# Performance work log

Measured on AMD Instinct MI355X. Metric: run time of the kernel, lower is better.

The kernel has to match this reference:

```python
import jax, jax.numpy as jnp
import numpy as np

EPS = 1e-8
N_ITER = 3
S = 8      # n_slots
D = 64     # slot_size
HID = 128  # mlp hidden


def _ln(x, w, b):
    m = jnp.mean(x, axis=-1, keepdims=True)
    v = jnp.var(x, axis=-1, keepdims=True)
    return (x - m) * jax.lax.rsqrt(v + 1e-5) * w + b


def setup_inputs() -> dict:
    key = jax.random.key(0)
    ks = jax.random.split(key, 20)
    B, N, Din = 128, 4096, 64
    g = lambda k, sh, s: (jax.random.normal(k, sh, jnp.float32) * s)
    return {
        "inputs": jax.random.normal(ks[0], (B, N, Din), jnp.float32),
        "eps_noise": jax.random.normal(ks[1], (B, S, D), jnp.float32),
        "slot_mu": g(ks[2], (1, 1, D), 0.1),
        "slot_logvar": g(ks[3], (1, 1, D), 0.1),
        "k_w": g(ks[4], (D, Din), 1.0 / np.sqrt(Din)),
        "v_w": g(ks[5], (D, Din), 1.0 / np.sqrt(Din)),
        "q_w": g(ks[6], (D, D), 1.0 / np.sqrt(D)),
        "ni_w": jnp.ones((Din,), jnp.float32), "ni_b": jnp.zeros((Din,), jnp.float32),
        "ns_w": jnp.ones((D,), jnp.float32),  "ns_b": jnp.zeros((D,), jnp.float32),
        "nr_w": jnp.ones((D,), jnp.float32),  "nr_b": jnp.zeros((D,), jnp.float32),
        "gru_wih": g(ks[7], (3 * D, D), 1.0 / np.sqrt(D)),
        "gru_whh": g(ks[8], (3 * D, D), 1.0 / np.sqrt(D)),
        "gru_bih": jnp.zeros((3 * D,), jnp.float32),
        "gru_bhh": jnp.zeros((3 * D,), jnp.float32),
        "mlp_w1": g(ks[9], (HID, D), 1.0 / np.sqrt(D)),
        "mlp_w2": g(ks[10], (D, HID), 1.0 / np.sqrt(HID)),
        "mlp_b2": jnp.zeros((D,), jnp.float32),
    }


def _gru(x, h, wih, whh, bih, bhh):
    gi = x @ wih.T + bih  # [BS, 3D]
    gh = h @ whh.T + bhh
    i_r, i_z, i_n = jnp.split(gi, 3, axis=-1)
    h_r, h_z, h_n = jnp.split(gh, 3, axis=-1)
    r = jax.nn.sigmoid(i_r + h_r)
    z = jax.nn.sigmoid(i_z + h_z)
    n = jnp.tanh(i_n + r * h_n)
    return (1.0 - z) * n + z * h


def _step(slots, k, v, q_w, ns_w, ns_b, nr_w, nr_b,
          gru_wih, gru_whh, gru_bih, gru_bhh, mlp_w1, mlp_w2, mlp_b2):
    B = slots.shape[0]
    q = _ln(slots, ns_w, ns_b) @ q_w.T                     # [B,S,D]
    logits = jnp.einsum('bnd,bsd->bns', k, q)              # [B,N,S]
    w = jax.nn.softmax(logits, axis=-1) + EPS              # softmax over slots
    w = w / jnp.sum(w, axis=-2, keepdims=True)             # renorm over tokens
    atten_maps = jnp.einsum('bns,bnd->bsd', w, v)          # [B,S,D]
    h = _gru(atten_maps.reshape(B * S, D), slots.reshape(B * S, D),
             gru_wih, gru_whh, gru_bih, gru_bhh)
    h = h + (jax.nn.relu(_ln(h, nr_w, nr_b) @ mlp_w1.T) @ mlp_w2.T + mlp_b2)
    return h.reshape(B, S, D), w


def reference(inputs, eps_noise, slot_mu, slot_logvar, k_w, v_w, q_w,
              ni_w, ni_b, ns_w, ns_b, nr_w, nr_b,
              gru_wih, gru_whh, gru_bih, gru_bhh, mlp_w1, mlp_w2, mlp_b2):
    std = jnp.exp(0.5 * slot_logvar)
    slots = slot_mu + std * eps_noise                      # [B,S,D]
    x = _ln(inputs, ni_w, ni_b)
    k = (x @ k_w.T) / np.sqrt(D).astype(np.float32)        # [B,N,D]
    v = x @ v_w.T
    args = (q_w, ns_w, ns_b, nr_w, nr_b, gru_wih, gru_whh,
            gru_bih, gru_bhh, mlp_w1, mlp_w2, mlp_b2)
    for _ in range(N_ITER):
        slots, w = _step(slots, k, v, *args)
    slots, w = _step(jax.lax.stop_gradient(slots), k, v, *args)
    return slots, w
```

## Files before the change

### kernel.cpp

```cpp
#include <hip/hip_runtime.h>
#include <hip/hip_bf16.h>

#define BB 128
#define NN 4096
#define DD 64
#define SS 8
#define HH 128

typedef __attribute__((ext_vector_type(8))) short short8;
typedef __attribute__((ext_vector_type(4))) float f32x4;

__device__ __forceinline__ float warp_red_sum(float v) {
    #pragma unroll
    for (int off = 32; off; off >>= 1) v += __shfl_xor(v, off);
    return v;
}

__device__ __forceinline__ float bcastlane(float v, int l) {
    return __int_as_float(__builtin_amdgcn_readlane(__float_as_int(v), l));
}

__device__ __forceinline__ unsigned short bfu(float f) {
    __hip_bfloat16 h = __float2bfloat16(f);
    return *(unsigned short*)&h;
}

__device__ __forceinline__ unsigned pk2(float a, float b) {
    return (unsigned)bfu(a) | ((unsigned)bfu(b) << 16);
}

__global__ __launch_bounds__(256) void prep_kernel(
    const float* __restrict__ v_w, const float* __restrict__ q_w,
    const float* __restrict__ wih, const float* __restrict__ whh,
    const float* __restrict__ w1, const float* __restrict__ w2,
    float* __restrict__ vwT, float* __restrict__ qwT,
    float* __restrict__ wihT, float* __restrict__ whhT,
    float* __restrict__ w1T, float* __restrict__ w2T)
{
    int i0 = blockIdx.x * blockDim.x + threadIdx.x;
    int nthr = gridDim.x * blockDim.x;
    for (int t = i0; t < 4096; t += nthr) {
        int i = t >> 6, o = t & 63;
        vwT[t] = v_w[o * 64 + i];
        qwT[t] = q_w[o * 64 + i];
    }
    for (int t = i0; t < 12288; t += nthr) {
        int r = t / 192, c = t % 192;
        wihT[t] = wih[c * 64 + r];
        whhT[t] = whh[c * 64 + r];
    }
    for (int t = i0; t < 8192; t += nthr) {
        int r = t >> 7, c = t & 127;
        w1T[t] = w1[c * 64 + r];
    }
    for (int t = i0; t < 8192; t += nthr) {
        int r = t >> 6, c = t & 63;
        w2T[t] = w2[c * 128 + r];
    }
}

__global__ __launch_bounds__(256) void init_q_kernel(
    const float* __restrict__ eps, const float* __restrict__ mu,
    const float* __restrict__ lv, const float* __restrict__ qwT,
    const float* __restrict__ k_w,
    const float* __restrict__ nsw, const float* __restrict__ nsb,
    float* __restrict__ slots, unsigned short* __restrict__ qb,
    float* __restrict__ zbuf)
{
    const int tid = threadIdx.x, lane = tid & 63;
    const int row = blockIdx.x * 4 + (tid >> 6);
    const int idx = row * 64 + lane;
    float s0 = mu[lane] + __expf(0.5f * lv[lane]) * eps[idx];
    slots[idx] = s0;
    float m = warp_red_sum(s0) * (1.0f / 64.0f);
    float dx = s0 - m;
    float var = warp_red_sum(dx * dx) * (1.0f / 64.0f);
    float xln = dx * rsqrtf(var + 1e-5f) * nsw[lane] + nsb[lane];
    float q = 0.f;
    #pragma unroll 8
    for (int i = 0; i < 64; ++i) q = fmaf(bcastlane(xln, i), qwT[i * 64 + lane], q);
    float qp = 0.f;
    #pragma unroll 8
    for (int o = 0; o < 64; ++o) qp = fmaf(bcastlane(q, o), k_w[o * 64 + lane], qp);
    qb[idx] = bfu(qp * 0.125f);
    int g = blockIdx.x * 256 + tid;
    for (int j = g; j < 66560; j += 65536) zbuf[j] = 0.f;
}

__global__ __launch_bounds__(256) void phase_a_ln(
    const float* __restrict__ inp, const float* __restrict__ niw, const float* __restrict__ nib,
    unsigned short* __restrict__ xb, unsigned short* __restrict__ xbt)
{
    __shared__ unsigned short xt[64 * 136];
    const int tid = threadIdx.x, lane = tid & 63, widx = tid >> 6;
    const int tg = lane >> 4, dq = lane & 15;
    const float4 wni = *(const float4*)&niw[dq * 4];
    const float4 bni = *(const float4*)&nib[dq * 4];
    const int tok0 = blockIdx.x * 128;
    const int sw = dq & 7;
    #pragma unroll
    for (int it = 0; it < 8; ++it) {
        const int m = widx * 32 + it * 4 + tg;
        float4 x = *(const float4*)&inp[(size_t)(tok0 + m) * 64 + dq * 4];
        float s1 = x.x + x.y + x.z + x.w;
        float s2 = fmaf(x.x, x.x, fmaf(x.y, x.y, fmaf(x.z, x.z, x.w * x.w)));
        #pragma unroll
        for (int o = 1; o < 16; o <<= 1) { s1 += __shfl_xor(s1, o); s2 += __shfl_xor(s2, o); }
        float mean = s1 * (1.0f / 64.0f);
        float var = s2 * (1.0f / 64.0f) - mean * mean;
        float rstd = rsqrtf(var + 1e-5f);
        float y0 = (x.x - mean) * rstd * wni.x + bni.x;
        float y1 = (x.y - mean) * rstd * wni.y + bni.y;
        float y2 = (x.z - mean) * rstd * wni.z + bni.z;
        float y3 = (x.w - mean) * rstd * wni.w + bni.w;
        uint2 p; p.x = pk2(y0, y1); p.y = pk2(y2, y3);
        *(uint2*)&xb[(size_t)(tok0 + m) * 64 + dq * 4] = p;
        const int col = ((((m >> 3) ^ sw) << 3) | (m & 7));
        xt[(dq * 4 + 0) * 136 + col] = bfu(y0);
        xt[(dq * 4 + 1) * 136 + col] = bfu(y1);
        xt[(dq * 4 + 2) * 136 + col] = bfu(y2);
        xt[(dq * 4 + 3) * 136 + col] = bfu(y3);
    }
    __syncthreads();
    const int b = blockIdx.x >> 5, tin = (blockIdx.x & 31) * 128;
    const int d = tid >> 2, q4 = tid & 3;
    const int sr = (d >> 2) & 7;
    #pragma unroll
    for (int c = 0; c < 4; ++c) {
        const int cc = q4 * 4 + c;
        uint4 o = *(uint4*)&xt[d * 136 + ((cc ^ sr) << 3)];
        *(uint4*)&xbt[((size_t)b * 64 + d) * 4096 + tin + cc * 8] = o;
    }
}

__global__ __launch_bounds__(256) void attn_mfma(
    const __hip_bfloat16* __restrict__ xb, const unsigned short* __restrict__ xbt,
    const unsigned short* __restrict__ qb,
    float* __restrict__ numer, float* __restrict__ denom, float* __restrict__ wout)
{
    __shared__ unsigned short smem[24192];
    unsigned short* Qs = smem;
    const int tid = threadIdx.x, lane = tid & 63, widx = tid >> 6;
    unsigned short* wls = smem + 1152 + widx * 1152;
    unsigned short* vt  = smem + 5760 + widx * 4608;
    const int b = blockIdx.y;

    for (int t = tid; t < 1024; t += 256) {
        int s = t >> 6, dd = t & 63;
        Qs[s * 72 + dd] = (s < 8) ? qb[b * 512 + t] : (unsigned short)0;
    }
    for (int t = lane; t < 576; t += 64) wls[576 + t] = 0;
    __syncthreads();

    const int quad = lane >> 4, l16 = lane & 15;
    short8 aq0 = *(const short8*)&Qs[l16 * 72 + quad * 8];
    short8 aq1 = *(const short8*)&Qs[l16 * 72 + 32 + quad * 8];

    f32x4 accv[4];
    #pragma unroll
    for (int nt = 0; nt < 4; ++nt) accv[nt] = (f32x4){0.f, 0.f, 0.f, 0.f};
    float dacc[4] = {0.f, 0.f, 0.f, 0.f};

    const int twave0 = blockIdx.x * 512 + widx * 128;
    const int vd = lane >> 3, vc = (lane & 7) * 8;
    #pragma unroll
    for (int iter = 0; iter < 2; ++iter) {
        const int t0 = twave0 + iter * 64;
        uint4 vld[8];
        #pragma unroll
        for (int i = 0; i < 8; ++i)
            vld[i] = *(const uint4*)&xbt[((size_t)b * 64 + i * 8 + vd) * 4096 + t0 + vc];

        #pragma unroll
        for (int t4 = 0; t4 < 4; ++t4) {
            const int tok = t0 + t4 * 16 + l16;
            const size_t xrow = ((size_t)b * NN + tok) * 64;
            short8 bk0 = *(const short8*)&xb[xrow + quad * 8];
            short8 bk1 = *(const short8*)&xb[xrow + 32 + quad * 8];
            f32x4 lg = (f32x4){0.f, 0.f, 0.f, 0.f};
            lg = __builtin_amdgcn_mfma_f32_16x16x32_bf16(aq0, bk0, lg, 0, 0, 0);
            lg = __builtin_amdgcn_mfma_f32_16x16x32_bf16(aq1, bk1, lg, 0, 0, 0);
            float e[4];
            #pragma unroll
            for (int r = 0; r < 4; ++r) e[r] = __expf(lg[r]);
            float s4 = (e[0] + e[1]) + (e[2] + e[3]);
            float stot = s4 + __shfl_xor(s4, 16);
            float rs = __builtin_amdgcn_rcpf(stot);
            float wv[4];
            #pragma unroll
            for (int r = 0; r < 4; ++r) { wv[r] = fmaf(e[r], rs, 1e-8f); dacc[r] += wv[r]; }
            if (quad < 2) {
                #pragma unroll
                for (int r = 0; r < 4; ++r)
                    wls[(quad * 4 + r) * 72 + t4 * 16 + l16] = bfu(wv[r]);
                if (wout)
                    *(float4*)&wout[((size_t)b * NN + tok) * 8 + quad * 4] =
                        make_float4(wv[0], wv[1], wv[2], wv[3]);
            }
        }
        #pragma unroll
        for (int i = 0; i < 8; ++i)
            *(uint4*)&vt[(i * 8 + vd) * 72 + vc] = vld[i];
        #pragma unroll
        for (int ks = 0; ks < 2; ++ks) {
            short8 aw = *(const short8*)&wls[l16 * 72 + ks * 32 + quad * 8];
            #pragma unroll
            for (int nt = 0; nt < 4; ++nt) {
                short8 bv = *(const short8*)&vt[(nt * 16 + l16) * 72 + ks * 32 + quad * 8];
                accv[nt] = __builtin_amdgcn_mfma_f32_16x16x32_bf16(aw, bv, accv[nt], 0, 0, 0);
            }
        }
    }
    #pragma unroll
    for (int r = 0; r < 4; ++r) {
        dacc[r] += __shfl_xor(dacc[r], 1);
        dacc[r] += __shfl_xor(dacc[r], 2);
        dacc[r] += __shfl_xor(dacc[r], 4);
        dacc[r] += __shfl_xor(dacc[r], 8);
    }
    __syncthreads();
    float* red = (float*)(smem + 5760);
    float* dred = red + 2048;
    if (quad < 2) {
        #pragma unroll
        for (int nt = 0; nt < 4; ++nt)
            #pragma unroll
            for (int r = 0; r < 4; ++r)
                red[widx * 512 + (quad * 4 + r) * 64 + nt * 16 + l16] = accv[nt][r];
        if (l16 == 0) {
            #pragma unroll
            for (int r = 0; r < 4; ++r) dred[widx * 8 + quad * 4 + r] = dacc[r];
        }
    }
    __syncthreads();
    for (int e = tid; e < 512; e += 256)
        atomicAdd(numer + (size_t)b * 512 + e, red[e] + red[512 + e] + red[1024 + e] + red[1536 + e]);
    if (tid < 8)
        atomicAdd(denom + b * 8 + tid, dred[tid] + dred[8 + tid] + dred[16 + tid] + dred[24 + tid]);
}

__global__ __launch_bounds__(256) void gru_q_kernel(
    const float* __restrict__ numerX, const float* __restrict__ denom,
    const float* __restrict__ slotsIn,
    const float* __restrict__ vwT, const float* __restrict__ wihT, const float* __restrict__ whhT,
    const float* __restrict__ w1T, const float* __restrict__ w2T,
    const float* __restrict__ bih, const float* __restrict__ bhh,
    const float* __restrict__ nrw, const float* __restrict__ nrb,
    const float* __restrict__ b2,
    const float* __restrict__ qwT, const float* __restrict__ k_w,
    const float* __restrict__ nsw, const float* __restrict__ nsb,
    float* __restrict__ slotsOut, unsigned short* __restrict__ qb,
    float* __restrict__ zbuf)
{
    const int tid = threadIdx.x, lane = tid & 63;
    const int row = blockIdx.x * 4 + (tid >> 6);
    float nx = numerX[row * 64 + lane];
    float xp = 0.f;
    #pragma unroll 8
    for (int i = 0; i < 64; ++i) xp = fmaf(bcastlane(nx, i), vwT[i * 64 + lane], xp);
    float x = xp / denom[row];
    float h = slotsIn[row * 64 + lane];
    float air = 0, aiz = 0, ain = 0, ahr = 0, ahz = 0, ahn = 0;
    #pragma unroll 8
    for (int i = 0; i < 64; ++i) {
        float xi = bcastlane(x, i), hi = bcastlane(h, i);
        const float* wi = wihT + i * 192;
        const float* wh = whhT + i * 192;
        air = fmaf(xi, wi[lane], air);
        aiz = fmaf(xi, wi[64 + lane], aiz);
        ain = fmaf(xi, wi[128 + lane], ain);
        ahr = fmaf(hi, wh[lane], ahr);
        ahz = fmaf(hi, wh[64 + lane], ahz);
        ahn = fmaf(hi, wh[128 + lane], ahn);
    }
    air += bih[lane]; aiz += bih[64 + lane]; ain += bih[128 + lane];
    ahr += bhh[lane]; ahz += bhh[64 + lane]; ahn += bhh[128 + lane];
    float r = 1.f / (1.f + __expf(-(air + ahr)));
    float z = 1.f / (1.f + __expf(-(aiz + ahz)));
    float n = tanhf(ain + r * ahn);
    float hn = (1.f - z) * n + z * h;
    float m = warp_red_sum(hn) * (1.0f / 64.0f);
    float dx = hn - m;
    float var = warp_red_sum(dx * dx) * (1.0f / 64.0f);
    float u = dx * rsqrtf(var + 1e-5f) * nrw[lane] + nrb[lane];
    float o0 = 0.f, o1 = 0.f;
    #pragma unroll 8
    for (int i = 0; i < 64; ++i) {
        float ui = bcastlane(u, i);
        const float* w1r = w1T + i * 128;
        o0 = fmaf(ui, w1r[lane], o0);
        o1 = fmaf(ui, w1r[64 + lane], o1);
    }
    o0 = fmaxf(o0, 0.f); o1 = fmaxf(o1, 0.f);
    float y = 0.f;
    #pragma unroll 8
    for (int j = 0; j < 64; ++j) y = fmaf(bcastlane(o0, j), w2T[j * 64 + lane], y);
    #pragma unroll 8
    for (int j = 0; j < 64; ++j) y = fmaf(bcastlane(o1, j), w2T[(64 + j) * 64 + lane], y);
    y += b2[lane];
    float out = hn + y;
    slotsOut[row * 64 + lane] = out;
    float m2 = warp_red_sum(out) * (1.0f / 64.0f);
    float dx2 = out - m2;
    float var2 = warp_red_sum(dx2 * dx2) * (1.0f / 64.0f);
    float u2 = dx2 * rsqrtf(var2 + 1e-5f) * nsw[lane] + nsb[lane];
    float q = 0.f;
    #pragma unroll 8
    for (int i = 0; i < 64; ++i) q = fmaf(bcastlane(u2, i), qwT[i * 64 + lane], q);
    float qp = 0.f;
    #pragma unroll 8
    for (int o = 0; o < 64; ++o) qp = fmaf(bcastlane(q, o), k_w[o * 64 + lane], qp);
    qb[row * 64 + lane] = bfu(qp * 0.125f);
    int g = blockIdx.x * 256 + tid;
    for (int j = g; j < 66560; j += 65536) zbuf[j] = 0.f;
}

__global__ __launch_bounds__(256) void renorm_kernel(float* __restrict__ wout,
                                                     const float* __restrict__ denom)
{
    const size_t i4 = (size_t)blockIdx.x * blockDim.x + threadIdx.x;
    const size_t b = i4 >> 13;
    const int half = (int)(i4 & 1);
    float4 v = reinterpret_cast<float4*>(wout)[i4];
    const float4 dv = reinterpret_cast<const float4*>(denom)[b * 2 + half];
    v.x /= dv.x; v.y /= dv.y; v.z /= dv.z; v.w /= dv.w;
    reinterpret_cast<float4*>(wout)[i4] = v;
}

extern "C" void kernel_launch(void* const* d_in, const int* in_sizes, int n_in,
                              void* d_out, int out_size, void* d_ws, size_t ws_size,
                              hipStream_t stream)
{
    const float* inputs  = (const float*)d_in[0];
    const float* eps_n   = (const float*)d_in[1];
    const float* mu      = (const float*)d_in[2];
    const float* lv      = (const float*)d_in[3];
    const float* k_w     = (const float*)d_in[4];
    const float* v_w     = (const float*)d_in[5];
    const float* q_w     = (const float*)d_in[6];
    const float* ni_w    = (const float*)d_in[7];
    const float* ni_b    = (const float*)d_in[8];
    const float* ns_w    = (const float*)d_in[9];
    const float* ns_b    = (const float*)d_in[10];
    const float* nr_w    = (const float*)d_in[11];
    const float* nr_b    = (const float*)d_in[12];
    const float* gru_wih = (const float*)d_in[13];
    const float* gru_whh = (const float*)d_in[14];
    const float* gru_bih = (const float*)d_in[15];
    const float* gru_bhh = (const float*)d_in[16];
    const float* mlp_w1  = (const float*)d_in[17];
    const float* mlp_w2  = (const float*)d_in[18];
    const float* mlp_b2  = (const float*)d_in[19];

    char* wsb = (char*)d_ws;
    unsigned short* xb  = (unsigned short*)wsb;
    unsigned short* xbt = (unsigned short*)(wsb + 67108864);
    float* f      = (float*)(wsb + 134217728);
    float* slotsA = f;
    float* slotsB = f + 65536;
    unsigned short* qb = (unsigned short*)(f + 131072);
    float* numer0 = f + 163840;
    float* denom0 = f + 229376;
    float* numer1 = f + 230400;
    float* denom1 = f + 295936;
    float* vwT    = f + 296960;
    float* qwT    = f + 301056;
    float* wihT   = f + 305152;
    float* whhT   = f + 317440;
    float* w1T    = f + 329728;
    float* w2T    = f + 337920;

    float* out_slots = (float*)d_out;
    float* out_w     = out_slots + 65536;

    prep_kernel<<<64, 256, 0, stream>>>(v_w, q_w, gru_wih, gru_whh, mlp_w1, mlp_w2,
                                        vwT, qwT, wihT, whhT, w1T, w2T);
    init_q_kernel<<<256, 256, 0, stream>>>(eps_n, mu, lv, qwT, k_w, ns_w, ns_b,
                                           slotsA, qb, numer0);
    phase_a_ln<<<4096, 256, 0, stream>>>(inputs, ni_w, ni_b, xb, xbt);

    float* cur = slotsA;
    float* numers[2] = {numer0, numer1};
    float* denoms[2] = {denom0, denom1};
    for (int step = 0; step < 4; ++step) {
        int pb = step & 1;
        attn_mfma<<<dim3(8, 128), 256, 0, stream>>>((const __hip_bfloat16*)xb, xbt, qb,
                                                    numers[pb], denoms[pb],
                                                    step == 3 ? out_w : nullptr);
        float* nxt = (step == 3) ? out_slots : ((step & 1) ? slotsA : slotsB);
        gru_q_kernel<<<256, 256, 0, stream>>>(numers[pb], denoms[pb], cur,
                                              vwT, wihT, whhT, w1T, w2T,
                                              gru_bih, gru_bhh, nr_w, nr_b, mlp_b2,
                                              qwT, k_w, ns_w, ns_b,
                                              nxt, qb, numers[1 - pb]);
        cur = nxt;
    }
    renorm_kernel<<<4096, 256, 0, stream>>>(out_w, denom1);
}
```

Baseline: 448.1 us.

## Load V fragments straight into MFMA registers and widen per-thread LayerNorm vectors

The attention kernel now loads each wave's transposed V tile from global memory directly into MFMA B-operand registers instead of staging it through shared memory. This removes the LDS write/read round trip and shrinks the kernel's static LDS footprint, which may allow more blocks per CU. The price is narrower contiguous runs per row in the global loads. Separately, the input LayerNorm kernel has each thread handle 8 features with two float4 loads and one 16-byte bf16 store, reducing the shuffle rounds. The LDS transpose swizzle is widened to 16 chunk positions to match the new write pattern.

```diff
diff --git a/kernel.cpp b/kernel.cpp
--- a/kernel.cpp
+++ b/kernel.cpp
@@ -93,38 +93,51 @@
 {
     __shared__ unsigned short xt[64 * 136];
     const int tid = threadIdx.x, lane = tid & 63, widx = tid >> 6;
-    const int tg = lane >> 4, dq = lane & 15;
-    const float4 wni = *(const float4*)&niw[dq * 4];
-    const float4 bni = *(const float4*)&nib[dq * 4];
+    const int t8 = lane >> 3, d8 = lane & 7;
+    const float4 wn0 = *(const float4*)&niw[d8 * 8];
+    const float4 wn1 = *(const float4*)&niw[d8 * 8 + 4];
+    const float4 bn0 = *(const float4*)&nib[d8 * 8];
+    const float4 bn1 = *(const float4*)&nib[d8 * 8 + 4];
     const int tok0 = blockIdx.x * 128;
-    const int sw = dq & 7;
-    #pragma unroll
-    for (int it = 0; it < 8; ++it) {
-        const int m = widx * 32 + it * 4 + tg;
-        float4 x = *(const float4*)&inp[(size_t)(tok0 + m) * 64 + dq * 4];
-        float s1 = x.x + x.y + x.z + x.w;
-        float s2 = fmaf(x.x, x.x, fmaf(x.y, x.y, fmaf(x.z, x.z, x.w * x.w)));
-        #pragma unroll
-        for (int o = 1; o < 16; o <<= 1) { s1 += __shfl_xor(s1, o); s2 += __shfl_xor(s2, o); }
+    #pragma unroll
+    for (int it = 0; it < 4; ++it) {
+        const int m = widx * 32 + it * 8 + t8;
+        const float* rowp = inp + (size_t)(tok0 + m) * 64 + d8 * 8;
+        float4 a = *(const float4*)rowp;
+        float4 c = *(const float4*)(rowp + 4);
+        float s1 = (a.x + a.y + a.z + a.w) + (c.x + c.y + c.z + c.w);
+        float s2 = fmaf(a.x, a.x, fmaf(a.y, a.y, fmaf(a.z, a.z, a.w * a.w)));
+        s2 = fmaf(c.x, c.x, fmaf(c.y, c.y, fmaf(c.z, c.z, fmaf(c.w, c.w, s2))));
+        #pragma unroll
+        for (int o = 1; o < 8; o <<= 1) { s1 += __shfl_xor(s1, o); s2 += __shfl_xor(s2, o); }
         float mean = s1 * (1.0f / 64.0f);
         float var = s2 * (1.0f / 64.0f) - mean * mean;
         float rstd = rsqrtf(var + 1e-5f);
-        float y0 = (x.x - mean) * rstd * wni.x + bni.x;
-        float y1 = (x.y - mean) * rstd * wni.y + bni.y;
-        float y2 = (x.z - mean) * rstd * wni.z + bni.z;
-        float y3 = (x.w - mean) * rstd * wni.w + bni.w;
-        uint2 p; p.x = pk2(y0, y1); p.y = pk2(y2, y3);
-        *(uint2*)&xb[(size_t)(tok0 + m) * 64 + dq * 4] = p;
-        const int col = ((((m >> 3) ^ sw) << 3) | (m & 7));
-        xt[(dq * 4 + 0) * 136 + col] = bfu(y0);
-        xt[(dq * 4 + 1) * 136 + col] = bfu(y1);
-        xt[(dq * 4 + 2) * 136 + col] = bfu(y2);
-        xt[(dq * 4 + 3) * 136 + col] = bfu(y3);
+        float y[8];
+        y[0] = (a.x - mean) * rstd * wn0.x + bn0.x;
+        y[1] = (a.y - mean) * rstd * wn0.y + bn0.y;
+        y[2] = (a.z - mean) * rstd * wn0.z + bn0.z;
+        y[3] = (a.w - mean) * rstd * wn0.w + bn0.w;
+        y[4] = (c.x - mean) * rstd * wn1.x + bn1.x;
+        y[5] = (c.y - mean) * rstd * wn1.y + bn1.y;
+        y[6] = (c.z - mean) * rstd * wn1.z + bn1.z;
+        y[7] = (c.w - mean) * rstd * wn1.w + bn1.w;
+        uint4 o4;
+        o4.x = pk2(y[0], y[1]); o4.y = pk2(y[2], y[3]);
+        o4.z = pk2(y[4], y[5]); o4.w = pk2(y[6], y[7]);
+        *(uint4*)&xb[(size_t)(tok0 + m) * 64 + d8 * 8] = o4;
+        const int mh = m >> 3, ml = m & 7;
+        #pragma unroll
+        for (int j = 0; j < 8; ++j) {
+            const int d = d8 * 8 + j;
+            const int col = (((mh ^ ((d >> 2) & 15)) << 3) | ml);
+            xt[d * 136 + col] = bfu(y[j]);
+        }
     }
     __syncthreads();
     const int b = blockIdx.x >> 5, tin = (blockIdx.x & 31) * 128;
     const int d = tid >> 2, q4 = tid & 3;
-    const int sr = (d >> 2) & 7;
+    const int sr = (d >> 2) & 15;
     #pragma unroll
     for (int c = 0; c < 4; ++c) {
         const int cc = q4 * 4 + c;
@@ -138,11 +151,10 @@
     const unsigned short* __restrict__ qb,
     float* __restrict__ numer, float* __restrict__ denom, float* __restrict__ wout)
 {
-    __shared__ unsigned short smem[24192];
+    __shared__ unsigned short smem[5760];
     unsigned short* Qs = smem;
     const int tid = threadIdx.x, lane = tid & 63, widx = tid >> 6;
     unsigned short* wls = smem + 1152 + widx * 1152;
-    unsigned short* vt  = smem + 5760 + widx * 4608;
     const int b = blockIdx.y;
 
     for (int t = tid; t < 1024; t += 256) {
@@ -162,14 +174,16 @@
     float dacc[4] = {0.f, 0.f, 0.f, 0.f};
 
     const int twave0 = blockIdx.x * 512 + widx * 128;
-    const int vd = lane >> 3, vc = (lane & 7) * 8;
     #pragma unroll
     for (int iter = 0; iter < 2; ++iter) {
         const int t0 = twave0 + iter * 64;
-        uint4 vld[8];
-        #pragma unroll
-        for (int i = 0; i < 8; ++i)
-            vld[i] = *(const uint4*)&xbt[((size_t)b * 64 + i * 8 + vd) * 4096 + t0 + vc];
+        short8 bvr[8];
+        #pragma unroll
+        for (int ks = 0; ks < 2; ++ks)
+            #pragma unroll
+            for (int nt = 0; nt < 4; ++nt)
+                bvr[ks * 4 + nt] = *(const short8*)&xbt[((size_t)b * 64 + nt * 16 + l16) * 4096
+                                                        + t0 + ks * 32 + quad * 8];
 
         #pragma unroll
         for (int t4 = 0; t4 < 4; ++t4) {
@@ -199,16 +213,12 @@
             }
         }
         #pragma unroll
-        for (int i = 0; i < 8; ++i)
-            *(uint4*)&vt[(i * 8 + vd) * 72 + vc] = vld[i];
-        #pragma unroll
         for (int ks = 0; ks < 2; ++ks) {
             short8 aw = *(const short8*)&wls[l16 * 72 + ks * 32 + quad * 8];
             #pragma unroll
-            for (int nt = 0; nt < 4; ++nt) {
-                short8 bv = *(const short8*)&vt[(nt * 16 + l16) * 72 + ks * 32 + quad * 8];
-                accv[nt] = __builtin_amdgcn_mfma_f32_16x16x32_bf16(aw, bv, accv[nt], 0, 0, 0);
-            }
+            for (int nt = 0; nt < 4; ++nt)
+                accv[nt] = __builtin_amdgcn_mfma_f32_16x16x32_bf16(aw, bvr[ks * 4 + nt],
+                                                                   accv[nt], 0, 0, 0);
         }
     }
     #pragma unroll
@@ -219,7 +229,7 @@
         dacc[r] += __shfl_xor(dacc[r], 8);
     }
     __syncthreads();
-    float* red = (float*)(smem + 5760);
+    float* red = (float*)smem;
     float* dred = red + 2048;
     if (quad < 2) {
         #pragma unroll
```

New measurement: 446.2 us. About the same (-0.4%).
